# Kernel tuning notes

Measured on AMD Instinct MI355X. Metric: run time of the kernel, lower is better.

## Reference

```python
import jax, jax.numpy as jnp
import numpy as np

C = 64  # in_dim

def _dwpw(x, w_dw, w_pw):
    # depthwise 1x1x1 conv (groups=C, no bias) == per-channel scale
    x = x * w_dw[None, :, None, None, None]
    # pointwise 1x1x1 conv (no bias) == channel mixing matmul
    return jnp.einsum('bcdhw,oc->bodhw', x, w_pw)

def setup_inputs() -> dict:
    key = jax.random.key(0)
    ks = jax.random.split(key, 8)
    B, D, H, W = 2, 16, 16, 16
    x = jax.random.normal(ks[0], (B, C, D, H, W), dtype=jnp.float32)
    s = 1.0 / np.sqrt(C)
    q_dw = jax.random.normal(ks[1], (C,), dtype=jnp.float32) * s
    q_pw = jax.random.normal(ks[2], (C, C), dtype=jnp.float32) * s
    k_dw = jax.random.normal(ks[3], (C,), dtype=jnp.float32) * s
    k_pw = jax.random.normal(ks[4], (C, C), dtype=jnp.float32) * s
    v_dw = jax.random.normal(ks[5], (C,), dtype=jnp.float32) * s
    v_pw = jax.random.normal(ks[6], (C, C), dtype=jnp.float32) * s
    gamma = jnp.zeros((1,), dtype=jnp.float32) + 0.1  # nonzero so output depends on attention
    return {"x": x, "q_dw": q_dw, "q_pw": q_pw, "k_dw": k_dw, "k_pw": k_pw,
            "v_dw": v_dw, "v_pw": v_pw, "gamma": gamma}

def reference(x, q_dw, q_pw, k_dw, k_pw, v_dw, v_pw, gamma):
    B, Cc, D, H, W = x.shape
    N = D * H * W
    q = _dwpw(x, q_dw, q_pw).reshape(B, Cc, N)  # [B,C,N]
    k = _dwpw(x, k_dw, k_pw).reshape(B, Cc, N)
    v = _dwpw(x, v_dw, v_pw).reshape(B, Cc, N)
    # energy[b,i,j] = sum_c q[b,c,i] * k[b,c,j]
    energy = jnp.einsum('bci,bcj->bij', q, k)
    attn = jax.nn.softmax(energy, axis=-1)  # softmax over j
    # out[b,c,i] = sum_j v[b,c,j] * attn[b,i,j]
    out = jnp.einsum('bcj,bij->bci', v, attn).reshape(B, Cc, D, H, W)
    return gamma * out + x
```

## Files before the change

### kernel.cpp

```cpp
#include <hip/hip_runtime.h>
#include <hip/hip_bf16.h>

#define NPOS 4096
#define CDIM 64
#define BATCH 2
#define JSPLIT 8
#define JSHIFT 3
#define JCHUNK (NPOS / JSPLIT)
#define NTILE (JCHUNK / 64)
#define RPB 128
#define PSTR 72

typedef __attribute__((ext_vector_type(8))) short bf16x8;
typedef __attribute__((ext_vector_type(4))) short short4b;
typedef __attribute__((ext_vector_type(4))) float f32x4;
typedef __attribute__((ext_vector_type(4))) unsigned int u32x4;
typedef __attribute__((ext_vector_type(2))) unsigned int u32x2;

static __device__ __forceinline__ unsigned int fbits(float f) {
    union { float f; unsigned int u; } v; v.f = f; return v.u;
}
static __device__ __forceinline__ float bffloat(unsigned int hi16) {
    union { unsigned int u; float f; } v; v.u = hi16; return v.f;
}
static __device__ __forceinline__ unsigned int pk2bf(float a, float b) {
    return ((fbits(a) + 0x8000u) >> 16) | ((fbits(b) + 0x8000u) & 0xffff0000u);
}
static __device__ __forceinline__ short f2bs(float f) {
    return (short)(unsigned short)((fbits(f) + 0x8000u) >> 16);
}

static __device__ __forceinline__ void gload16(const void* g, void* l) {
    __builtin_amdgcn_global_load_lds(
        (const __attribute__((address_space(1))) unsigned int*)g,
        (__attribute__((address_space(3))) unsigned int*)l, 16, 0, 0);
}

__global__ __launch_bounds__(64) void qkv_kernel(
    const float* __restrict__ x,
    const float* __restrict__ q_dw, const float* __restrict__ q_pw,
    const float* __restrict__ k_dw, const float* __restrict__ k_pw,
    const float* __restrict__ v_dw, const float* __restrict__ v_pw,
    short* __restrict__ qT, short* __restrict__ kT, short* __restrict__ vM)
{
    const int bid  = blockIdx.x;
    const int p    = bid >> 9;
    const int np   = bid & 511;
    const int b    = np >> 8;
    const int n0   = (np & 255) << 4;
    const int lane = threadIdx.x;
    const int col  = lane & 15;
    const int quad = lane >> 4;
    const int n    = n0 + col;

    const float* pw = (p == 0) ? q_pw : (p == 1) ? k_pw : v_pw;
    const float* dw = (p == 0) ? q_dw : (p == 1) ? k_dw : v_dw;

    bf16x8 xf0, xf1;
    float dv0[8], dv1[8];
    #pragma unroll
    for (int j = 0; j < 8; ++j) {
        xf0[j] = f2bs(x[(size_t)(b * CDIM + quad * 8 + j) * NPOS + n]);
        xf1[j] = f2bs(x[(size_t)(b * CDIM + 32 + quad * 8 + j) * NPOS + n]);
        dv0[j] = dw[quad * 8 + j];
        dv1[j] = dw[32 + quad * 8 + j];
    }

    #pragma unroll
    for (int os = 0; os < 4; ++os) {
        const float* pr = pw + (os * 16 + col) * 64 + quad * 8;
        bf16x8 wf0, wf1;
        #pragma unroll
        for (int j = 0; j < 8; ++j) {
            wf0[j] = f2bs(pr[j] * dv0[j]);
            wf1[j] = f2bs(pr[32 + j] * dv1[j]);
        }
        f32x4 d = (f32x4){0.f, 0.f, 0.f, 0.f};
        if (p < 2) {
            d = __builtin_amdgcn_mfma_f32_16x16x32_bf16(wf0, xf0, d, 0, 0, 0);
            d = __builtin_amdgcn_mfma_f32_16x16x32_bf16(wf1, xf1, d, 0, 0, 0);
            short* dst = p ? kT : qT;
            *(u32x2*)(dst + (size_t)(b * NPOS + n) * CDIM + os * 16 + quad * 4) =
                (u32x2){pk2bf(d[0], d[1]), pk2bf(d[2], d[3])};
        } else {
            d = __builtin_amdgcn_mfma_f32_16x16x32_bf16(xf0, wf0, d, 0, 0, 0);
            d = __builtin_amdgcn_mfma_f32_16x16x32_bf16(xf1, wf1, d, 0, 0, 0);
            *(u32x2*)(vM + (size_t)(b * CDIM + os * 16 + col) * NPOS + n0 + quad * 4) =
                (u32x2){pk2bf(d[0], d[1]), pk2bf(d[2], d[3])};
        }
    }
}

__global__ __launch_bounds__(256, 2) void attn_kernel(
    const short* __restrict__ qT, const short* __restrict__ kT,
    const short* __restrict__ vM,
    unsigned short* __restrict__ Opart, float* __restrict__ lacc)
{
    const int gid  = blockIdx.x;
    const int jc   = gid & (JSPLIT - 1);
    const int rb   = (gid >> JSHIFT) & 31;
    const int b    = gid >> (JSHIFT + 5);
    const int t    = threadIdx.x;
    const int wave = t >> 6;
    const int lane = t & 63;
    const int col  = lane & 15;
    const int quad = lane >> 4;

    __shared__ __align__(16) short Kbuf[2][64 * 64];
    __shared__ __align__(16) short Vbuf[2][64 * 64];
    __shared__ __align__(16) short Pw[4][32 * PSTR];

    const short* qTb = qT + (size_t)b * NPOS * CDIM;
    const char*  kTB = (const char*)(kT + (size_t)b * NPOS * CDIM);
    const char*  vB  = (const char*)(vM + (size_t)b * CDIM * NPOS);

    const int i0 = rb * RPB + wave * 32;

    auto stage = [&](int tt) {
        const int j0 = jc * JCHUNK + tt * 64;
        const char* kS = kTB + (size_t)j0 * (CDIM * 2);
        const char* vS = vB  + (size_t)j0 * 2;
        char* kD = (char*)&Kbuf[tt & 1][0];
        char* vD = (char*)&Vbuf[tt & 1][0];
        #pragma unroll
        for (int i = 0; i < 2; ++i) {
            const int base = wave * 2048 + i * 1024;
            const int L    = base + lane * 16;
            const int r    = L >> 7;
            const int o    = (L & 127) ^ ((r & 7) << 4);
            gload16(kS + (size_t)((L & ~127) + o), kD + base);
            gload16(vS + (size_t)r * (NPOS * 2) + o, vD + base);
        }
    };

    bf16x8 qf[2][2];
    #pragma unroll
    for (int rs = 0; rs < 2; ++rs) {
        const short* qp = qTb + (size_t)(i0 + rs * 16 + col) * CDIM + quad * 8;
        qf[rs][0] = *(const bf16x8*)qp;
        qf[rs][1] = *(const bf16x8*)(qp + 32);
    }

    f32x4 oacc[2][4];
    #pragma unroll
    for (int rs = 0; rs < 2; ++rs)
        #pragma unroll
        for (int cb = 0; cb < 4; ++cb) oacc[rs][cb] = (f32x4){0.f, 0.f, 0.f, 0.f};
    float lp[2] = {0.f, 0.f};

    short* Pme = Pw[wave];
    const int slot = (quad * 16) ^ ((col & 7) << 4);

    stage(0);
    __syncthreads();

    for (int tt = 0; tt < NTILE; ++tt) {
        if (tt + 1 < NTILE) stage(tt + 1);

        const char* Kc = (const char*)&Kbuf[tt & 1][0];
        const char* Vc = (const char*)&Vbuf[tt & 1][0];

        #pragma unroll
        for (int ct = 0; ct < 4; ++ct) {
            const char* kr = Kc + (ct * 16 + col) * 128;
            bf16x8 k0 = *(const bf16x8*)(kr + slot);
            bf16x8 k1 = *(const bf16x8*)(kr + (slot ^ 64));
            #pragma unroll
            for (int rs = 0; rs < 2; ++rs) {
                f32x4 a = (f32x4){0.f, 0.f, 0.f, 0.f};
                a = __builtin_amdgcn_mfma_f32_16x16x32_bf16(k0, qf[rs][0], a, 0, 0, 0);
                a = __builtin_amdgcn_mfma_f32_16x16x32_bf16(k1, qf[rs][1], a, 0, 0, 0);
                float p0 = __expf(a[0]), p1 = __expf(a[1]);
                float p2 = __expf(a[2]), p3 = __expf(a[3]);
                lp[rs] += (p0 + p1) + (p2 + p3);
                *(short4b*)(Pme + (rs * 16 + col) * PSTR + ct * 16 + quad * 4) =
                    (short4b){f2bs(p0), f2bs(p1), f2bs(p2), f2bs(p3)};
            }
        }

        bf16x8 pf[2][2];
        #pragma unroll
        for (int rs = 0; rs < 2; ++rs) {
            const short* pp = Pme + (rs * 16 + col) * PSTR + quad * 8;
            pf[rs][0] = *(const bf16x8*)pp;
            pf[rs][1] = *(const bf16x8*)(pp + 32);
        }

        #pragma unroll
        for (int cb = 0; cb < 4; ++cb) {
            const char* vr = Vc + (cb * 16 + col) * 128;
            bf16x8 v0 = *(const bf16x8*)(vr + slot);
            bf16x8 v1 = *(const bf16x8*)(vr + (slot ^ 64));
            #pragma unroll
            for (int rs = 0; rs < 2; ++rs) {
                oacc[rs][cb] = __builtin_amdgcn_mfma_f32_16x16x32_bf16(v0, pf[rs][0], oacc[rs][cb], 0, 0, 0);
                oacc[rs][cb] = __builtin_amdgcn_mfma_f32_16x16x32_bf16(v1, pf[rs][1], oacc[rs][cb], 0, 0, 0);
            }
        }
        __syncthreads();
    }

    #pragma unroll
    for (int rs = 0; rs < 2; ++rs) {
        lp[rs] += __shfl_xor(lp[rs], 16, 64);
        lp[rs] += __shfl_xor(lp[rs], 32, 64);
    }
    if (quad == 0) {
        #pragma unroll
        for (int rs = 0; rs < 2; ++rs)
            lacc[(size_t)(jc * BATCH + b) * NPOS + i0 + rs * 16 + col] = lp[rs];
    }

    unsigned short* Ob = Opart + (size_t)(jc * BATCH + b) * CDIM * NPOS;
    #pragma unroll
    for (int rs = 0; rs < 2; ++rs)
        #pragma unroll
        for (int cb = 0; cb < 4; ++cb)
            #pragma unroll
            for (int r = 0; r < 4; ++r)
                Ob[(size_t)(cb * 16 + quad * 4 + r) * NPOS + i0 + rs * 16 + col] =
                    (unsigned short)f2bs(oacc[rs][cb][r]);
}

__global__ __launch_bounds__(256) void combine_kernel(
    const unsigned short* __restrict__ Opart, const float* __restrict__ lacc,
    const float* __restrict__ x, const float* __restrict__ gamma,
    float* __restrict__ out)
{
    int b  = blockIdx.x >> 7;
    int n0 = (blockIdx.x & 127) << 5;
    __shared__ float linv[32];
    int t = threadIdx.x;
    if (t < 32) {
        float s = 0.f;
        #pragma unroll
        for (int jc = 0; jc < JSPLIT; ++jc)
            s += lacc[(size_t)(jc * BATCH + b) * NPOS + n0 + t];
        linv[t] = gamma[0] / s;
    }
    __syncthreads();

    int c = t >> 2, ns = (t & 3) * 8;
    float acc[8];
    #pragma unroll
    for (int k = 0; k < 8; ++k) acc[k] = 0.f;
    #pragma unroll
    for (int jc = 0; jc < JSPLIT; ++jc) {
        const unsigned short* Ob = Opart + ((size_t)(jc * BATCH + b) * CDIM + c) * NPOS + n0 + ns;
        u32x4 w = *(const u32x4*)Ob;
        #pragma unroll
        for (int j = 0; j < 4; ++j) {
            acc[2 * j]     += bffloat(w[j] << 16);
            acc[2 * j + 1] += bffloat(w[j] & 0xffff0000u);
        }
    }
    const float* xb = x + ((size_t)b * CDIM + c) * NPOS + n0 + ns;
    float* ob = out + ((size_t)b * CDIM + c) * NPOS + n0 + ns;
    #pragma unroll
    for (int k = 0; k < 2; ++k) {
        f32x4 x4 = *(const f32x4*)(xb + k * 4);
        f32x4 r;
        #pragma unroll
        for (int j = 0; j < 4; ++j)
            r[j] = fmaf(acc[k * 4 + j], linv[ns + k * 4 + j], x4[j]);
        *(f32x4*)(ob + k * 4) = r;
    }
}

extern "C" void kernel_launch(void* const* d_in, const int* in_sizes, int n_in,
                              void* d_out, int out_size, void* d_ws, size_t ws_size,
                              hipStream_t stream) {
    const float* x     = (const float*)d_in[0];
    const float* q_dw  = (const float*)d_in[1];
    const float* q_pw  = (const float*)d_in[2];
    const float* k_dw  = (const float*)d_in[3];
    const float* k_pw  = (const float*)d_in[4];
    const float* v_dw  = (const float*)d_in[5];
    const float* v_pw  = (const float*)d_in[6];
    const float* gamma = (const float*)d_in[7];
    float* out = (float*)d_out;

    char* ws = (char*)d_ws;
    short* qT             = (short*)(ws);
    short* kT             = (short*)(ws + (1u << 20));
    short* vM             = (short*)(ws + (2u << 20));
    unsigned short* Opart = (unsigned short*)(ws + (3u << 20));
    float* lacc           = (float*)(ws + (3u << 20) +
                                     (size_t)JSPLIT * BATCH * CDIM * NPOS * 2);

    qkv_kernel<<<3 * BATCH * 256, 64, 0, stream>>>(
        x, q_dw, q_pw, k_dw, k_pw, v_dw, v_pw, qT, kT, vM);
    attn_kernel<<<BATCH * 32 * JSPLIT, 256, 0, stream>>>(qT, kT, vM, Opart, lacc);
    combine_kernel<<<BATCH * 128, 256, 0, stream>>>(Opart, lacc, x, gamma, out);
}
```

Before: 97.54 us.

## Halve rows per attention block, raise occupancy, swizzle P buffer and set MFMA priority

Each wave in the attention kernel now handles 16 query rows instead of 32, so a block covers 64 rows and the grid doubles to 1024 blocks. Launch bounds allow 4 blocks per CU. The padded P scratch buffer is replaced by an unpadded 64-wide layout with XOR swizzling, and s_setprio is raised around the MFMA calls. This trades K/V reuse per staged tile, since each K/V tile is now loaded for half as many rows, for more parallelism and lower register and LDS pressure.

```diff
diff --git a/kernel.cpp b/kernel.cpp
--- a/kernel.cpp
+++ b/kernel.cpp
@@ -8,8 +8,7 @@
 #define JSHIFT 3
 #define JCHUNK (NPOS / JSPLIT)
 #define NTILE (JCHUNK / 64)
-#define RPB 128
-#define PSTR 72
+#define RPB 64
 
 typedef __attribute__((ext_vector_type(8))) short bf16x8;
 typedef __attribute__((ext_vector_type(4))) short short4b;
@@ -91,15 +90,15 @@
     }
 }
 
-__global__ __launch_bounds__(256, 2) void attn_kernel(
+__global__ __launch_bounds__(256, 4) void attn_kernel(
     const short* __restrict__ qT, const short* __restrict__ kT,
     const short* __restrict__ vM,
     unsigned short* __restrict__ Opart, float* __restrict__ lacc)
 {
     const int gid  = blockIdx.x;
     const int jc   = gid & (JSPLIT - 1);
-    const int rb   = (gid >> JSHIFT) & 31;
-    const int b    = gid >> (JSHIFT + 5);
+    const int rb   = (gid >> JSHIFT) & 63;
+    const int b    = gid >> (JSHIFT + 6);
     const int t    = threadIdx.x;
     const int wave = t >> 6;
     const int lane = t & 63;
@@ -108,13 +107,13 @@
 
     __shared__ __align__(16) short Kbuf[2][64 * 64];
     __shared__ __align__(16) short Vbuf[2][64 * 64];
-    __shared__ __align__(16) short Pw[4][32 * PSTR];
+    __shared__ __align__(16) short Pw[4][16 * 64];
 
     const short* qTb = qT + (size_t)b * NPOS * CDIM;
     const char*  kTB = (const char*)(kT + (size_t)b * NPOS * CDIM);
     const char*  vB  = (const char*)(vM + (size_t)b * CDIM * NPOS);
 
-    const int i0 = rb * RPB + wave * 32;
+    const int i0 = rb * RPB + wave * 16;
 
     auto stage = [&](int tt) {
         const int j0 = jc * JCHUNK + tt * 64;
@@ -133,23 +132,21 @@
         }
     };
 
-    bf16x8 qf[2][2];
-    #pragma unroll
-    for (int rs = 0; rs < 2; ++rs) {
-        const short* qp = qTb + (size_t)(i0 + rs * 16 + col) * CDIM + quad * 8;
-        qf[rs][0] = *(const bf16x8*)qp;
-        qf[rs][1] = *(const bf16x8*)(qp + 32);
-    }
-
-    f32x4 oacc[2][4];
-    #pragma unroll
-    for (int rs = 0; rs < 2; ++rs)
-        #pragma unroll
-        for (int cb = 0; cb < 4; ++cb) oacc[rs][cb] = (f32x4){0.f, 0.f, 0.f, 0.f};
-    float lp[2] = {0.f, 0.f};
-
-    short* Pme = Pw[wave];
-    const int slot = (quad * 16) ^ ((col & 7) << 4);
+    bf16x8 qf[2];
+    {
+        const short* qp = qTb + (size_t)(i0 + col) * CDIM + quad * 8;
+        qf[0] = *(const bf16x8*)qp;
+        qf[1] = *(const bf16x8*)(qp + 32);
+    }
+
+    f32x4 oacc[4];
+    #pragma unroll
+    for (int cb = 0; cb < 4; ++cb) oacc[cb] = (f32x4){0.f, 0.f, 0.f, 0.f};
+    float lp = 0.f;
+
+    char* Pc = (char*)&Pw[wave][0];
+    const int pswz = (col & 7) << 4;
+    const int slot = (quad * 16) ^ pswz;
 
     stage(0);
     __syncthreads();
@@ -165,61 +162,46 @@
             const char* kr = Kc + (ct * 16 + col) * 128;
             bf16x8 k0 = *(const bf16x8*)(kr + slot);
             bf16x8 k1 = *(const bf16x8*)(kr + (slot ^ 64));
-            #pragma unroll
-            for (int rs = 0; rs < 2; ++rs) {
-                f32x4 a = (f32x4){0.f, 0.f, 0.f, 0.f};
-                a = __builtin_amdgcn_mfma_f32_16x16x32_bf16(k0, qf[rs][0], a, 0, 0, 0);
-                a = __builtin_amdgcn_mfma_f32_16x16x32_bf16(k1, qf[rs][1], a, 0, 0, 0);
-                float p0 = __expf(a[0]), p1 = __expf(a[1]);
-                float p2 = __expf(a[2]), p3 = __expf(a[3]);
-                lp[rs] += (p0 + p1) + (p2 + p3);
-                *(short4b*)(Pme + (rs * 16 + col) * PSTR + ct * 16 + quad * 4) =
-                    (short4b){f2bs(p0), f2bs(p1), f2bs(p2), f2bs(p3)};
-            }
-        }
-
-        bf16x8 pf[2][2];
-        #pragma unroll
-        for (int rs = 0; rs < 2; ++rs) {
-            const short* pp = Pme + (rs * 16 + col) * PSTR + quad * 8;
-            pf[rs][0] = *(const bf16x8*)pp;
-            pf[rs][1] = *(const bf16x8*)(pp + 32);
-        }
+            f32x4 a = (f32x4){0.f, 0.f, 0.f, 0.f};
+            __builtin_amdgcn_s_setprio(1);
+            a = __builtin_amdgcn_mfma_f32_16x16x32_bf16(k0, qf[0], a, 0, 0, 0);
+            a = __builtin_amdgcn_mfma_f32_16x16x32_bf16(k1, qf[1], a, 0, 0, 0);
+            __builtin_amdgcn_s_setprio(0);
+            float p0 = __expf(a[0]), p1 = __expf(a[1]);
+            float p2 = __expf(a[2]), p3 = __expf(a[3]);
+            lp += (p0 + p1) + (p2 + p3);
+            *(short4b*)(Pc + col * 128 + ((ct * 32 + quad * 8) ^ pswz)) =
+                (short4b){f2bs(p0), f2bs(p1), f2bs(p2), f2bs(p3)};
+        }
+
+        bf16x8 pf0 = *(const bf16x8*)(Pc + col * 128 + slot);
+        bf16x8 pf1 = *(const bf16x8*)(Pc + col * 128 + (slot ^ 64));
 
         #pragma unroll
         for (int cb = 0; cb < 4; ++cb) {
             const char* vr = Vc + (cb * 16 + col) * 128;
             bf16x8 v0 = *(const bf16x8*)(vr + slot);
             bf16x8 v1 = *(const bf16x8*)(vr + (slot ^ 64));
-            #pragma unroll
-            for (int rs = 0; rs < 2; ++rs) {
-                oacc[rs][cb] = __builtin_amdgcn_mfma_f32_16x16x32_bf16(v0, pf[rs][0], oacc[rs][cb], 0, 0, 0);
-                oacc[rs][cb] = __builtin_amdgcn_mfma_f32_16x16x32_bf16(v1, pf[rs][1], oacc[rs][cb], 0, 0, 0);
-            }
+            __builtin_amdgcn_s_setprio(1);
+            oacc[cb] = __builtin_amdgcn_mfma_f32_16x16x32_bf16(v0, pf0, oacc[cb], 0, 0, 0);
+            oacc[cb] = __builtin_amdgcn_mfma_f32_16x16x32_bf16(v1, pf1, oacc[cb], 0, 0, 0);
+            __builtin_amdgcn_s_setprio(0);
         }
         __syncthreads();
     }
 
-    #pragma unroll
-    for (int rs = 0; rs < 2; ++rs) {
-        lp[rs] += __shfl_xor(lp[rs], 16, 64);
-        lp[rs] += __shfl_xor(lp[rs], 32, 64);
-    }
-    if (quad == 0) {
-        #pragma unroll
-        for (int rs = 0; rs < 2; ++rs)
-            lacc[(size_t)(jc * BATCH + b) * NPOS + i0 + rs * 16 + col] = lp[rs];
-    }
+    lp += __shfl_xor(lp, 16, 64);
+    lp += __shfl_xor(lp, 32, 64);
+    if (quad == 0)
+        lacc[(size_t)(jc * BATCH + b) * NPOS + i0 + col] = lp;
 
     unsigned short* Ob = Opart + (size_t)(jc * BATCH + b) * CDIM * NPOS;
     #pragma unroll
-    for (int rs = 0; rs < 2; ++rs)
-        #pragma unroll
-        for (int cb = 0; cb < 4; ++cb)
-            #pragma unroll
-            for (int r = 0; r < 4; ++r)
-                Ob[(size_t)(cb * 16 + quad * 4 + r) * NPOS + i0 + rs * 16 + col] =
-                    (unsigned short)f2bs(oacc[rs][cb][r]);
+    for (int cb = 0; cb < 4; ++cb)
+        #pragma unroll
+        for (int r = 0; r < 4; ++r)
+            Ob[(size_t)(cb * 16 + quad * 4 + r) * NPOS + i0 + col] =
+                (unsigned short)f2bs(oacc[cb][r]);
 }
 
 __global__ __launch_bounds__(256) void combine_kernel(
@@ -290,6 +272,6 @@
 
     qkv_kernel<<<3 * BATCH * 256, 64, 0, stream>>>(
         x, q_dw, q_pw, k_dw, k_pw, v_dw, v_pw, qT, kT, vM);
-    attn_kernel<<<BATCH * 32 * JSPLIT, 256, 0, stream>>>(qT, kT, vM, Opart, lacc);
+    attn_kernel<<<BATCH * (NPOS / RPB) * JSPLIT, 256, 0, stream>>>(qT, kT, vM, Opart, lacc);
     combine_kernel<<<BATCH * 128, 256, 0, stream>>>(Opart, lacc, x, gamma, out);
 }
```

Result: no change. 97.47 us (-0.1%).
